# Kernel tuning notes

Hardware: AMD Instinct MI355X
Metric: run time of the kernel (lower is better)

Reference implementation:

```python
import jax, jax.numpy as jnp
import numpy as np

D_MODEL = 512
PROJ = 2 * D_MODEL  # 1024
N_STATES = 32
KSIZE = 4
LN_EPS = 1e-3  # keras LayerNormalization default epsilon


def setup_inputs() -> dict:
    key = jax.random.key(0)
    ks = jax.random.split(key, 16)
    B, L = 2, 2048
    s_in = 1.0 / np.sqrt(D_MODEL)
    s_pr = 1.0 / np.sqrt(PROJ)
    x = jax.random.normal(ks[0], (B, L, D_MODEL), dtype=jnp.float32)
    # LayerNorm params
    ln_gamma = jnp.ones((D_MODEL,), jnp.float32)
    ln_beta = jnp.zeros((D_MODEL,), jnp.float32)
    # dense1 / dense2: d_model -> proj
    W1 = jax.random.normal(ks[1], (D_MODEL, PROJ), jnp.float32) * s_in
    b1 = jnp.zeros((PROJ,), jnp.float32)
    W2 = jax.random.normal(ks[2], (D_MODEL, PROJ), jnp.float32) * s_in
    b2 = jnp.zeros((PROJ,), jnp.float32)
    # depthwise causal conv1d: kernel (K, 1, PROJ) in WIO layout, groups=PROJ
    conv_k = jax.random.normal(ks[3], (KSIZE, 1, PROJ), jnp.float32) * 0.5
    conv_b = jnp.zeros((PROJ,), jnp.float32)
    # SSM params
    A_log = jnp.log(jnp.broadcast_to(jnp.arange(1, N_STATES + 1, dtype=jnp.float32), (PROJ, N_STATES)))
    D_skip = jnp.ones((PROJ,), jnp.float32)
    WB = jax.random.normal(ks[4], (PROJ, N_STATES), jnp.float32) * s_pr
    bB = jnp.zeros((N_STATES,), jnp.float32)
    WC = jax.random.normal(ks[5], (PROJ, N_STATES), jnp.float32) * s_pr
    bC = jnp.zeros((N_STATES,), jnp.float32)
    Wd = jax.random.normal(ks[6], (PROJ, PROJ), jnp.float32) * s_pr
    bd = jnp.zeros((PROJ,), jnp.float32)
    # dense3: proj -> d_model
    W3 = jax.random.normal(ks[7], (PROJ, D_MODEL), jnp.float32) * s_pr
    b3 = jnp.zeros((D_MODEL,), jnp.float32)
    return dict(x=x, ln_gamma=ln_gamma, ln_beta=ln_beta, W1=W1, b1=b1, W2=W2, b2=b2,
                conv_k=conv_k, conv_b=conv_b, A_log=A_log, D_skip=D_skip,
                WB=WB, bB=bB, WC=WC, bC=bC, Wd=Wd, bd=bd, W3=W3, b3=b3)


def _layernorm(x, gamma, beta):
    mu = jnp.mean(x, axis=-1, keepdims=True)
    var = jnp.mean(jnp.square(x - mu), axis=-1, keepdims=True)
    return (x - mu) * jax.lax.rsqrt(var + LN_EPS) * gamma + beta


def _causal_dwconv(x, k, b):
    # x: [B,L,C], k: [K,1,C], depthwise causal conv (left-pad K-1)
    y = jax.lax.conv_general_dilated(
        x, k, window_strides=(1,), padding=[(KSIZE - 1, 0)],
        dimension_numbers=('NWC', 'WIO', 'NWC'), feature_group_count=PROJ)
    return y + b


def _selective_scan(u, delta, A, Bm, Cm, D_skip):
    # u, delta: [B,L,D]; A: [D,N]; Bm, Cm: [B,L,N]; D_skip: [D]
    deltaA = jnp.einsum('bld,dn->bldn', delta, A)                 # [B,L,D,N]
    deltaBu = jnp.einsum('bld,bld,bln->bldn', delta, u, Bm)        # [B,L,D,N]
    # shift deltaA left by one along L, zero at the end (pad trick in source)
    shifted = jnp.concatenate([deltaA[:, 1:], jnp.zeros_like(deltaA[:, :1])], axis=1)
    # reversed cumsum along L, then exp
    e = jnp.exp(jnp.flip(jnp.cumsum(jnp.flip(shifted, axis=1), axis=1), axis=1))
    xs = jnp.cumsum(deltaBu * e, axis=1) / (e + 1e-12)
    y = jnp.einsum('bldn,bln->bld', xs, Cm)
    return y + u * D_skip


def reference(x, ln_gamma, ln_beta, W1, b1, W2, b2, conv_k, conv_b,
              A_log, D_skip, WB, bB, WC, bC, Wd, bd, W3, b3):
    h = _layernorm(x, ln_gamma, ln_beta)
    x1 = h @ W1 + b1                      # [B,L,PROJ]
    x1 = _causal_dwconv(x1, conv_k, conv_b)
    x1 = jax.nn.silu(x1)
    A = -jnp.exp(A_log)                    # [PROJ,N]
    Cm = x1 @ WC + bC                      # [B,L,N]
    Bm = x1 @ WB + bB                      # [B,L,N]
    delta = jax.nn.softplus(x1 @ Wd + bd)  # [B,L,PROJ]
    y = _selective_scan(x1, delta, A, Bm, Cm, D_skip)
    x2 = jax.nn.silu(h @ W2 + b2)
    out = (y * x2) @ W3 + b3 + x           # residual; dropout is identity at inference
    return out
```

## Files before the change

### kernel.cpp

```cpp
#include <hip/hip_runtime.h>
#include <stdint.h>

#define L_SEQ 2048
#define BATCH 2
#define DMODEL 512
#define PROJ 1024
#define NST 32
#define NCATU 1088
#define ROWS (BATCH*L_SEQ)
#define THRESH 50.0f

typedef float f32x4 __attribute__((ext_vector_type(4)));
typedef short short8 __attribute__((ext_vector_type(8)));

__device__ inline float bf2f(unsigned short u){ uint32_t x=((uint32_t)u)<<16; float f; __builtin_memcpy(&f,&x,4); return f; }
__device__ inline unsigned short f2bf(float f){ uint32_t x; __builtin_memcpy(&x,&f,4); uint32_t r=x+0x7FFFu+((x>>16)&1u); return (unsigned short)(r>>16); }
__device__ inline float siluf(float x){ return x/(1.f+__expf(-x)); }
__device__ inline float softplusf(float x){ return x>20.f? x : log1pf(__expf(x)); }

#define AS1(p) ((const __attribute__((address_space(1))) void*)(p))
#define AS3(p) ((__attribute__((address_space(3))) void*)(p))

template<int N> __device__ inline void wait_vmcnt(){
  if constexpr (N==0)      asm volatile("s_waitcnt vmcnt(0)" ::: "memory");
  else if constexpr (N==4) asm volatile("s_waitcnt vmcnt(4)" ::: "memory");
  else if constexpr (N==8) asm volatile("s_waitcnt vmcnt(8)" ::: "memory");
  else                     asm volatile("s_waitcnt vmcnt(12)" ::: "memory");
}

__global__ __launch_bounds__(256)
void prep_ln_kernel(const float* __restrict__ W1, const float* __restrict__ b1,
                    const float* __restrict__ W2, const float* __restrict__ b2,
                    const float* __restrict__ Wd, const float* __restrict__ bd,
                    const float* __restrict__ WB, const float* __restrict__ bB,
                    const float* __restrict__ WC, const float* __restrict__ bC,
                    const float* __restrict__ W3,
                    unsigned short* __restrict__ W12t, unsigned short* __restrict__ Wcatt,
                    unsigned short* __restrict__ W3t, float* __restrict__ bias12,
                    float* __restrict__ biascat,
                    const float* __restrict__ x, const float* __restrict__ ln_g,
                    const float* __restrict__ ln_b, unsigned short* __restrict__ H)
{
  __shared__ float tile[32][33];
  int bid = blockIdx.x;
  int lx = threadIdx.x & 31, ly = threadIdx.x >> 5;
  if (bid < 1024) {
    int kt = bid & 15, nt = bid >> 4;
    int k0 = kt*32, n0 = nt*32;
    const float* S = (n0 < 1024) ? W1 : W2;
    int nc = (n0 < 1024) ? n0 : n0 - 1024;
#pragma unroll
    for (int i=0;i<4;i++)
      tile[ly+i*8][lx] = S[(size_t)(k0+ly+i*8)*1024 + nc + lx];
    __syncthreads();
#pragma unroll
    for (int i=0;i<4;i++)
      W12t[(size_t)(n0+ly+i*8)*512 + k0 + lx] = f2bf(tile[lx][ly+i*8]);
    return;
  }
  if (bid < 2112) {
    int t = bid - 1024;
    int kt = t & 31, nt = t >> 5;
    int k0 = kt*32, n0 = nt*32;
#pragma unroll
    for (int i=0;i<4;i++){
      int k = k0 + ly + i*8;
      float v;
      if (n0 < 1024)       v = Wd[(size_t)k*1024 + n0 + lx];
      else if (n0 == 1024) v = WB[(size_t)k*32 + lx];
      else                 v = WC[(size_t)k*32 + lx];
      tile[ly+i*8][lx] = v;
    }
    __syncthreads();
#pragma unroll
    for (int i=0;i<4;i++)
      Wcatt[(size_t)(n0+ly+i*8)*1024 + k0 + lx] = f2bf(tile[lx][ly+i*8]);
    return;
  }
  if (bid < 2624) {
    int t = bid - 2112;
    int kt = t & 31, nt = t >> 5;
    int k0 = kt*32, n0 = nt*32;
#pragma unroll
    for (int i=0;i<4;i++)
      tile[ly+i*8][lx] = W3[(size_t)(k0+ly+i*8)*512 + n0 + lx];
    __syncthreads();
#pragma unroll
    for (int i=0;i<4;i++)
      W3t[(size_t)(n0+ly+i*8)*1024 + k0 + lx] = f2bf(tile[lx][ly+i*8]);
    return;
  }
  if (bid < 2637) {
    int j = (bid - 2624)*256 + threadIdx.x;
    if (j < 2048) { bias12[j] = (j < 1024) ? b1[j] : b2[j-1024]; return; }
    j -= 2048;
    if (j < NCATU) biascat[j] = (j < 1024) ? bd[j] : (j < 1056) ? bB[j-1024] : bC[j-1056];
    return;
  }
  int row = (bid - 2637)*4 + (threadIdx.x >> 6);
  int lane = threadIdx.x & 63;
  const float4* xr = (const float4*)(x + (size_t)row*DMODEL);
  float4 v0 = xr[lane];
  float4 v1 = xr[lane+64];
  float s = v0.x+v0.y+v0.z+v0.w + v1.x+v1.y+v1.z+v1.w;
  float q = v0.x*v0.x+v0.y*v0.y+v0.z*v0.z+v0.w*v0.w
          + v1.x*v1.x+v1.y*v1.y+v1.z*v1.z+v1.w*v1.w;
#pragma unroll
  for (int m=32;m>0;m>>=1){ s += __shfl_xor(s,m); q += __shfl_xor(q,m); }
  float mu = s*(1.f/DMODEL);
  float var = q*(1.f/DMODEL) - mu*mu;
  float rs = rsqrtf(var + 1e-3f);
  int c0 = lane*4, c1 = 256 + lane*4;
  float4 g0 = *(const float4*)&ln_g[c0]; float4 g1 = *(const float4*)&ln_g[c1];
  float4 t0 = *(const float4*)&ln_b[c0]; float4 t1 = *(const float4*)&ln_b[c1];
  ushort4 o0, o1;
  o0.x = f2bf((v0.x-mu)*rs*g0.x + t0.x);
  o0.y = f2bf((v0.y-mu)*rs*g0.y + t0.y);
  o0.z = f2bf((v0.z-mu)*rs*g0.z + t0.z);
  o0.w = f2bf((v0.w-mu)*rs*g0.w + t0.w);
  o1.x = f2bf((v1.x-mu)*rs*g1.x + t1.x);
  o1.y = f2bf((v1.y-mu)*rs*g1.y + t1.y);
  o1.z = f2bf((v1.z-mu)*rs*g1.z + t1.z);
  o1.w = f2bf((v1.w-mu)*rs*g1.w + t1.w);
  *(ushort4*)&H[(size_t)row*DMODEL + c0] = o0;
  *(ushort4*)&H[(size_t)row*DMODEL + c1] = o1;
}

__global__ __launch_bounds__(256)
void gemm128_g1(const unsigned short* __restrict__ A, const unsigned short* __restrict__ Bt,
                unsigned short* __restrict__ P12n, unsigned short* __restrict__ x2bf,
                const float* __restrict__ bias, int M, int N, int K)
{
  constexpr int BK = 64;
  constexpr int LPT = 8;
  __shared__ unsigned short As[2][128*BK];
  __shared__ unsigned short Bs[2][128*BK];
  int tid = threadIdx.x;
  int lane = tid & 63, wid = tid >> 6;
  int wm = wid >> 1, wn = wid & 1;
  int gx = gridDim.x;
  int nwg = gx * gridDim.y;
  int L = blockIdx.y*gx + blockIdx.x;
  int W = (L & 7)*(nwg >> 3) + (L >> 3);
  int bx = W % gx, by = W / gx;
  int m0 = bx*128, n0 = by*128;

  f32x4 acc[4][4];
#pragma unroll
  for (int i=0;i<4;i++)
#pragma unroll
    for (int j=0;j<4;j++)
#pragma unroll
      for (int e=0;e<4;e++) acc[i][j][e] = 0.f;

  const unsigned short* ap[4];
  const unsigned short* bp[4];
#pragma unroll
  for (int j=0;j<4;j++){
    int s = tid + j*256;
    int row = s >> 3, kc = ((s & 7) ^ (row & 7)) * 8;
    ap[j] = A + (size_t)(m0+row)*K + kc;
    bp[j] = Bt + (size_t)(n0+row)*K + kc;
  }
  auto stage = [&](int buf){
#pragma unroll
    for (int j=0;j<4;j++){
      __builtin_amdgcn_global_load_lds(AS1(ap[j]), AS3(&As[buf][(size_t)(j*256 + wid*64)*8]), 16, 0, 0);
      ap[j] += BK;
    }
#pragma unroll
    for (int j=0;j<4;j++){
      __builtin_amdgcn_global_load_lds(AS1(bp[j]), AS3(&Bs[buf][(size_t)(j*256 + wid*64)*8]), 16, 0, 0);
      bp[j] += BK;
    }
  };
  stage(0);
  stage(1);
  int T = K/BK;
  int r = lane & 15, kb = lane >> 4;
  for (int t = 0; t < T; ++t) {
    int rb = t & 1;
    if (t+1 < T) wait_vmcnt<LPT>();
    else         wait_vmcnt<0>();
    __builtin_amdgcn_s_barrier();
    short8 af[2][4], bfr[2][4];
#pragma unroll
    for (int ks=0; ks<2; ++ks) {
      int cx = (ks*4 + kb) ^ (r & 7);
#pragma unroll
      for (int i=0;i<4;i++) af[ks][i]  = *(const short8*)&As[rb][((wm*64 + i*16 + r)*8 + cx)*8];
#pragma unroll
      for (int j=0;j<4;j++) bfr[ks][j] = *(const short8*)&Bs[rb][((wn*64 + j*16 + r)*8 + cx)*8];
    }
    asm volatile("s_waitcnt lgkmcnt(0)" ::: "memory");
    __builtin_amdgcn_sched_barrier(0);
    __builtin_amdgcn_s_barrier();
    if (t+2 < T) stage(rb);
    __builtin_amdgcn_s_setprio(1);
#pragma unroll
    for (int ks=0; ks<2; ++ks)
#pragma unroll
      for (int i=0;i<4;i++)
#pragma unroll
        for (int j=0;j<4;j++)
          acc[i][j] = __builtin_amdgcn_mfma_f32_16x16x32_bf16(af[ks][i], bfr[ks][j], acc[i][j], 0,0,0);
    __builtin_amdgcn_s_setprio(0);
  }

  int rr = (lane >> 4)*4, cc = lane & 15;
#pragma unroll
  for (int i=0;i<4;i++)
#pragma unroll
    for (int j=0;j<4;j++) {
      int col = n0 + wn*64 + j*16 + cc;
      float bcol = bias[col];
#pragma unroll
      for (int e=0;e<4;e++) {
        int row = m0 + wm*64 + i*16 + rr + e;
        float v = acc[i][j][e] + bcol;
        if (col < 1024) P12n[(size_t)row*1024 + col] = f2bf(v);
        else            x2bf[(size_t)row*1024 + col - 1024] = f2bf(siluf(v));
      }
    }
}

template<int MODE>
__global__ __launch_bounds__(256)
void gemm64(const unsigned short* __restrict__ A, const unsigned short* __restrict__ Bt,
            void* __restrict__ Cv, const float* __restrict__ bias,
            int M, int N, int K, int Kfull)
{
  constexpr int BK = 64;
  constexpr int LPT = 4;
  __shared__ unsigned short As[3][64*BK];
  __shared__ unsigned short Bs[3][64*BK];
  int tid = threadIdx.x;
  int lane = tid & 63, wid = tid >> 6;
  int wm = wid >> 1, wn = wid & 1;
  int gx = gridDim.x;
  int nwg = gx * gridDim.y;
  int L = blockIdx.y*gx + blockIdx.x;
  int W = (L & 7)*(nwg >> 3) + (L >> 3);
  int bx = W % gx, by = W / gx;
  int m0 = bx*64, n0 = by*64;
  int kofs = blockIdx.z*K;

  f32x4 acc[2][2];
#pragma unroll
  for (int i=0;i<2;i++)
#pragma unroll
    for (int j=0;j<2;j++)
#pragma unroll
      for (int e=0;e<4;e++) acc[i][j][e] = 0.f;

  const unsigned short* ap[2];
  const unsigned short* bp[2];
#pragma unroll
  for (int j=0;j<2;j++){
    int s = tid + j*256;
    int row = s >> 3, kc = ((s & 7) ^ (row & 7)) * 8;
    ap[j] = A + (size_t)(m0+row)*Kfull + kofs + kc;
    bp[j] = Bt + (size_t)(n0+row)*Kfull + kofs + kc;
  }
  auto stage = [&](int buf){
#pragma unroll
    for (int j=0;j<2;j++){
      __builtin_amdgcn_global_load_lds(AS1(ap[j]), AS3(&As[buf][(size_t)(j*256 + wid*64)*8]), 16, 0, 0);
      ap[j] += BK;
    }
#pragma unroll
    for (int j=0;j<2;j++){
      __builtin_amdgcn_global_load_lds(AS1(bp[j]), AS3(&Bs[buf][(size_t)(j*256 + wid*64)*8]), 16, 0, 0);
      bp[j] += BK;
    }
  };
  stage(0); stage(1);
  int T = K/BK;
  int rb = 0, wb = 2;
  int r = lane & 15, kb = lane >> 4;
  for (int t = 0; t < T; ++t) {
    if (t+1 < T) wait_vmcnt<LPT>();
    else         wait_vmcnt<0>();
    __builtin_amdgcn_s_barrier();
    if (t+2 < T) { stage(wb); wb = (wb==2)?0:wb+1; }
#pragma unroll
    for (int ks=0; ks<2; ++ks) {
      int cx = (ks*4 + kb) ^ (r & 7);
      short8 af[2], bfr[2];
#pragma unroll
      for (int i=0;i<2;i++) af[i]  = *(const short8*)&As[rb][((wm*32 + i*16 + r)*8 + cx)*8];
#pragma unroll
      for (int j=0;j<2;j++) bfr[j] = *(const short8*)&Bs[rb][((wn*32 + j*16 + r)*8 + cx)*8];
      __builtin_amdgcn_s_setprio(1);
#pragma unroll
      for (int i=0;i<2;i++)
#pragma unroll
        for (int j=0;j<2;j++)
          acc[i][j] = __builtin_amdgcn_mfma_f32_16x16x32_bf16(af[i], bfr[j], acc[i][j], 0,0,0);
      __builtin_amdgcn_s_setprio(0);
    }
    rb = (rb==2)?0:rb+1;
  }
  int rr = (lane >> 4)*4, cc = lane & 15;
#pragma unroll
  for (int i=0;i<2;i++)
#pragma unroll
    for (int j=0;j<2;j++) {
      int col = n0 + wn*32 + j*16 + cc;
#pragma unroll
      for (int e=0;e<4;e++) {
        int row = m0 + wm*32 + i*16 + rr + e;
        float v = acc[i][j][e];
        if constexpr (MODE == 2) {
          v += bias[row];
          if (row < 1024) v = softplusf(v);
          ((float*)Cv)[(size_t)row*N + col] = v;
        } else {
          ((float*)Cv)[(size_t)blockIdx.z*M*N + (size_t)row*N + col] = v;
        }
      }
    }
}

__global__ __launch_bounds__(256)
void reduce_kernel(const float* __restrict__ P, const float* __restrict__ x,
                   const float* __restrict__ b3, float* __restrict__ out)
{
  size_t i = ((size_t)blockIdx.x*256 + threadIdx.x)*4;
  int col = (int)(i & 511);
  float4 a = *(const float4*)&P[i];
  float4 b = *(const float4*)&P[(size_t)ROWS*512 + i];
  float4 xv = *(const float4*)&x[i];
  float4 bv = *(const float4*)&b3[col];
  float4 o;
  o.x = a.x + b.x + xv.x + bv.x;
  o.y = a.y + b.y + xv.y + bv.y;
  o.z = a.z + b.z + xv.z + bv.z;
  o.w = a.w + b.w + xv.w + bv.w;
  *(float4*)&out[i] = o;
}

__global__ __launch_bounds__(256)
void conv_silu_kernel(const unsigned short* __restrict__ P12n, const float* __restrict__ ck,
                      const float* __restrict__ cb, unsigned short* __restrict__ ubf)
{
  int gid = blockIdx.x*256 + threadIdx.x;
  int c = (gid & 255)*4;
  int row = gid >> 8;
  int l = row & (L_SEQ-1);
  float4 bv = *(const float4*)&cb[c];
  float r0=bv.x, r1=bv.y, r2=bv.z, r3=bv.w;
#pragma unroll
  for (int t=0;t<4;t++){
    int lsrc = l - 3 + t;
    if (lsrc >= 0) {
      ushort4 xv = *(const ushort4*)&P12n[(size_t)(row-3+t)*1024 + c];
      float4 kv = *(const float4*)&ck[t*PROJ + c];
      r0 = fmaf(bf2f(xv.x),kv.x,r0);
      r1 = fmaf(bf2f(xv.y),kv.y,r1);
      r2 = fmaf(bf2f(xv.z),kv.z,r2);
      r3 = fmaf(bf2f(xv.w),kv.w,r3);
    }
  }
  ushort4 o;
  o.x=f2bf(siluf(r0)); o.y=f2bf(siluf(r1)); o.z=f2bf(siluf(r2)); o.w=f2bf(siluf(r3));
  *(ushort4*)&ubf[(size_t)row*PROJ + c] = o;
}

__global__ __launch_bounds__(256)
void zmul_pre_kernel(const unsigned short* __restrict__ ubf, const unsigned short* __restrict__ x2bf,
                     const float* __restrict__ Dskip, unsigned short* __restrict__ zbf)
{
  size_t i = ((size_t)blockIdx.x*256 + threadIdx.x)*4;
  int d = (int)(i & (PROJ-1));
  ushort4 uu = *(const ushort4*)&ubf[i];
  ushort4 xx = *(const ushort4*)&x2bf[i];
  float4 Dv = *(const float4*)&Dskip[d];
  ushort4 o;
  o.x = f2bf(bf2f(uu.x)*Dv.x*bf2f(xx.x));
  o.y = f2bf(bf2f(uu.y)*Dv.y*bf2f(xx.y));
  o.z = f2bf(bf2f(uu.z)*Dv.z*bf2f(xx.z));
  o.w = f2bf(bf2f(uu.w)*Dv.w*bf2f(xx.w));
  *(ushort4*)&zbf[i] = o;
}

__global__ __launch_bounds__(256)
void sscan_kernel(const float* __restrict__ CT, const unsigned short* __restrict__ ubf,
                  const unsigned short* __restrict__ x2bf, const float* __restrict__ Dskip,
                  const float* __restrict__ A_log, unsigned short* __restrict__ zbf)
{
  __shared__ float suf8sh[8][256];
  int tid = threadIdx.x;
  int n = tid & 31, gsub = tid >> 5;
  int G = blockIdx.x*8 + gsub;
  int b = G >> 10, d = G & 1023;
  const float* dT = CT + (size_t)d*ROWS + b*L_SEQ;

  float mysum = 0.f;
  {
    const float4* c4 = (const float4*)(dT + n*64);
    for (int it=0; it<16; ++it){ float4 v = c4[it]; mysum += v.x+v.y+v.z+v.w; }
  }
  float incl = mysum;
#pragma unroll
  for (int dlt=1; dlt<32; dlt<<=1){ float t = __shfl_up(incl, dlt, 32); if (n >= dlt) incl += t; }
  float Tot = __shfl(incl, 31, 32);
  float excl = incl - mysum;
  int cnt = 0;
  {
    const float4* c4 = (const float4*)(dT + n*64);
    float run = excl;
    for (int it=0; it<16; ++it){
      float4 v = c4[it];
      if ((it & 1) == 0) suf8sh[gsub][n*8 + (it>>1)] = Tot - run;
      cnt += (Tot - run >= THRESH); run += v.x;
      cnt += (Tot - run >= THRESH); run += v.y;
      cnt += (Tot - run >= THRESH); run += v.z;
      cnt += (Tot - run >= THRESH); run += v.w;
    }
  }
#pragma unroll
  for (int m=16;m>0;m>>=1) cnt += __shfl_xor(cnt, m, 32);
  int myl0 = cnt > 0 ? cnt-1 : 0;
  __syncthreads();

  int base = min(myl0, __shfl_xor(myl0, 32)) & ~7;
  float np1 = __expf(A_log[d*NST + n]);
  float Ds = Dskip[d];
  const float* Br = CT + (size_t)(1024+n)*ROWS + b*L_SEQ;
  const float* Cr = CT + (size_t)(1056+n)*ROWS + b*L_SEQ;
  const unsigned short* ub = ubf + (size_t)b*L_SEQ*PROJ + d;
  const unsigned short* xb = x2bf + (size_t)b*L_SEQ*PROJ + d;
  unsigned short* zb = zbf + (size_t)b*L_SEQ*PROJ + d;
  float s = 0.f;
  for (int l = base; l < L_SEQ; l += 8) {
    float4 d0 = *(const float4*)&dT[l];
    float4 d1 = *(const float4*)&dT[l+4];
    float4 B0 = *(const float4*)&Br[l];
    float4 B1 = *(const float4*)&Br[l+4];
    float4 C0 = *(const float4*)&Cr[l];
    float4 C1 = *(const float4*)&Cr[l+4];
    float sufv = suf8sh[gsub][l >> 3];
    float dl[8] = {d0.x,d0.y,d0.z,d0.w,d1.x,d1.y,d1.z,d1.w};
    float Bv[8] = {B0.x,B0.y,B0.z,B0.w,B1.x,B1.y,B1.z,B1.w};
    float Cv[8] = {C0.x,C0.y,C0.z,C0.w,C1.x,C1.y,C1.z,C1.w};
    float uu[8];
#pragma unroll
    for (int t=0;t<8;t++) uu[t] = bf2f(ub[(size_t)(l+t)*PROJ]);
    float cum = 0.f;
#pragma unroll
    for (int t=0;t<8;t++){
      cum += dl[t];
      float decay = __expf(-dl[t]*np1);
      s = fmaf(decay, s, dl[t]*uu[t]*Bv[t]);
      float gte = 1.f/(1.f + 1e-12f*__expf(np1*(sufv - cum)));
      float contrib = s*gte*Cv[t];
#pragma unroll
      for (int m=16;m>0;m>>=1) contrib += __shfl_xor(contrib, m);
      if (n == 0) {
        float x2v = bf2f(xb[(size_t)(l+t)*PROJ]);
        zb[(size_t)(l+t)*PROJ] = f2bf((contrib + uu[t]*Ds)*x2v);
      }
    }
  }
}

extern "C" void kernel_launch(void* const* d_in, const int* in_sizes, int n_in,
                              void* d_out, int out_size, void* d_ws, size_t ws_size,
                              hipStream_t stream)
{
  const float* x     = (const float*)d_in[0];
  const float* ln_g  = (const float*)d_in[1];
  const float* ln_b  = (const float*)d_in[2];
  const float* W1    = (const float*)d_in[3];
  const float* b1    = (const float*)d_in[4];
  const float* W2    = (const float*)d_in[5];
  const float* b2    = (const float*)d_in[6];
  const float* convk = (const float*)d_in[7];
  const float* convb = (const float*)d_in[8];
  const float* A_log = (const float*)d_in[9];
  const float* Dskip = (const float*)d_in[10];
  const float* WB    = (const float*)d_in[11];
  const float* bB    = (const float*)d_in[12];
  const float* WC    = (const float*)d_in[13];
  const float* bC    = (const float*)d_in[14];
  const float* Wd    = (const float*)d_in[15];
  const float* bd    = (const float*)d_in[16];
  const float* W3    = (const float*)d_in[17];
  const float* b3    = (const float*)d_in[18];

  char* w = (char*)d_ws;
  auto alloc = [&](size_t bytes){ char* p = w; w += (bytes + 255) & ~(size_t)255; return p; };
  unsigned short* Hbf    = (unsigned short*)alloc((size_t)ROWS*DMODEL*2);
  unsigned short* W12t   = (unsigned short*)alloc((size_t)2048*512*2);
  unsigned short* Wcatt  = (unsigned short*)alloc((size_t)NCATU*1024*2);
  unsigned short* W3t    = (unsigned short*)alloc((size_t)512*1024*2);
  float*          bias12 = (float*)alloc(2048*4);
  float*          biascat= (float*)alloc(NCATU*4);
  unsigned short* P12n   = (unsigned short*)alloc((size_t)ROWS*1024*2);
  unsigned short* ubf    = (unsigned short*)alloc((size_t)ROWS*PROJ*2);
  unsigned short* x2bf   = (unsigned short*)alloc((size_t)ROWS*PROJ*2);
  float*          CT     = (float*)alloc((size_t)NCATU*ROWS*4);
  unsigned short* zbf    = (unsigned short*)alloc((size_t)ROWS*PROJ*2);
  float*          Pp     = (float*)alloc((size_t)2*ROWS*512*4);

  prep_ln_kernel<<<3661, 256, 0, stream>>>(W1,b1,W2,b2,Wd,bd,WB,bB,WC,bC,W3,
                                           W12t,Wcatt,W3t,bias12,biascat,
                                           x, ln_g, ln_b, Hbf);

  dim3 g1(ROWS/128, 2048/128);
  gemm128_g1<<<g1, 256, 0, stream>>>(Hbf, W12t, P12n, x2bf, bias12, ROWS, 2048, DMODEL);

  conv_silu_kernel<<<ROWS*256/256, 256, 0, stream>>>(P12n, convk, convb, ubf);

  zmul_pre_kernel<<<(ROWS*PROJ/4)/256, 256, 0, stream>>>(ubf, x2bf, Dskip, zbf);

  dim3 g2(NCATU/64, ROWS/64);
  gemm64<2><<<g2, 256, 0, stream>>>(Wcatt, ubf, CT, biascat, NCATU, ROWS, PROJ, PROJ);

  sscan_kernel<<<2048/8, 256, 0, stream>>>(CT, ubf, x2bf, Dskip, A_log, zbf);

  dim3 g3(ROWS/64, 512/64, 2);
  gemm64<5><<<g3, 256, 0, stream>>>(zbf, W3t, Pp, b3, ROWS, 512, 512, PROJ);
  reduce_kernel<<<(ROWS*512/4)/256, 256, 0, stream>>>(Pp, x, b3, (float*)d_out);
}
```

Before: 162.9 us.

## Run first projection GEMM with 64x64 tiles and hoist x2 loads in scan

Removes the dedicated 128x128-tile GEMM for the LN-to-W1/W2 projection and reuses the 64x64-tile gemm64 template with a new MODE 1 epilogue, which applies the bias, writes the conv input and silu(x2) in bf16, and launches four times as many workgroups. Separately, the selective-scan kernel now loads the eight x2 values per step up front alongside u instead of inside the n==0 branch of the inner loop. The smaller tile raises occupancy and CU coverage for a K=512 GEMM but lowers data reuse per tile. The hoisted loads are now issued by all lanes rather than only n==0 lanes, trading extra loads for less latency on the serial path.

```diff
diff --git a/kernel.cpp b/kernel.cpp
--- a/kernel.cpp
+++ b/kernel.cpp
@@ -126,108 +126,10 @@
   *(ushort4*)&H[(size_t)row*DMODEL + c1] = o1;
 }
 
-__global__ __launch_bounds__(256)
-void gemm128_g1(const unsigned short* __restrict__ A, const unsigned short* __restrict__ Bt,
-                unsigned short* __restrict__ P12n, unsigned short* __restrict__ x2bf,
-                const float* __restrict__ bias, int M, int N, int K)
-{
-  constexpr int BK = 64;
-  constexpr int LPT = 8;
-  __shared__ unsigned short As[2][128*BK];
-  __shared__ unsigned short Bs[2][128*BK];
-  int tid = threadIdx.x;
-  int lane = tid & 63, wid = tid >> 6;
-  int wm = wid >> 1, wn = wid & 1;
-  int gx = gridDim.x;
-  int nwg = gx * gridDim.y;
-  int L = blockIdx.y*gx + blockIdx.x;
-  int W = (L & 7)*(nwg >> 3) + (L >> 3);
-  int bx = W % gx, by = W / gx;
-  int m0 = bx*128, n0 = by*128;
-
-  f32x4 acc[4][4];
-#pragma unroll
-  for (int i=0;i<4;i++)
-#pragma unroll
-    for (int j=0;j<4;j++)
-#pragma unroll
-      for (int e=0;e<4;e++) acc[i][j][e] = 0.f;
-
-  const unsigned short* ap[4];
-  const unsigned short* bp[4];
-#pragma unroll
-  for (int j=0;j<4;j++){
-    int s = tid + j*256;
-    int row = s >> 3, kc = ((s & 7) ^ (row & 7)) * 8;
-    ap[j] = A + (size_t)(m0+row)*K + kc;
-    bp[j] = Bt + (size_t)(n0+row)*K + kc;
-  }
-  auto stage = [&](int buf){
-#pragma unroll
-    for (int j=0;j<4;j++){
-      __builtin_amdgcn_global_load_lds(AS1(ap[j]), AS3(&As[buf][(size_t)(j*256 + wid*64)*8]), 16, 0, 0);
-      ap[j] += BK;
-    }
-#pragma unroll
-    for (int j=0;j<4;j++){
-      __builtin_amdgcn_global_load_lds(AS1(bp[j]), AS3(&Bs[buf][(size_t)(j*256 + wid*64)*8]), 16, 0, 0);
-      bp[j] += BK;
-    }
-  };
-  stage(0);
-  stage(1);
-  int T = K/BK;
-  int r = lane & 15, kb = lane >> 4;
-  for (int t = 0; t < T; ++t) {
-    int rb = t & 1;
-    if (t+1 < T) wait_vmcnt<LPT>();
-    else         wait_vmcnt<0>();
-    __builtin_amdgcn_s_barrier();
-    short8 af[2][4], bfr[2][4];
-#pragma unroll
-    for (int ks=0; ks<2; ++ks) {
-      int cx = (ks*4 + kb) ^ (r & 7);
-#pragma unroll
-      for (int i=0;i<4;i++) af[ks][i]  = *(const short8*)&As[rb][((wm*64 + i*16 + r)*8 + cx)*8];
-#pragma unroll
-      for (int j=0;j<4;j++) bfr[ks][j] = *(const short8*)&Bs[rb][((wn*64 + j*16 + r)*8 + cx)*8];
-    }
-    asm volatile("s_waitcnt lgkmcnt(0)" ::: "memory");
-    __builtin_amdgcn_sched_barrier(0);
-    __builtin_amdgcn_s_barrier();
-    if (t+2 < T) stage(rb);
-    __builtin_amdgcn_s_setprio(1);
-#pragma unroll
-    for (int ks=0; ks<2; ++ks)
-#pragma unroll
-      for (int i=0;i<4;i++)
-#pragma unroll
-        for (int j=0;j<4;j++)
-          acc[i][j] = __builtin_amdgcn_mfma_f32_16x16x32_bf16(af[ks][i], bfr[ks][j], acc[i][j], 0,0,0);
-    __builtin_amdgcn_s_setprio(0);
-  }
-
-  int rr = (lane >> 4)*4, cc = lane & 15;
-#pragma unroll
-  for (int i=0;i<4;i++)
-#pragma unroll
-    for (int j=0;j<4;j++) {
-      int col = n0 + wn*64 + j*16 + cc;
-      float bcol = bias[col];
-#pragma unroll
-      for (int e=0;e<4;e++) {
-        int row = m0 + wm*64 + i*16 + rr + e;
-        float v = acc[i][j][e] + bcol;
-        if (col < 1024) P12n[(size_t)row*1024 + col] = f2bf(v);
-        else            x2bf[(size_t)row*1024 + col - 1024] = f2bf(siluf(v));
-      }
-    }
-}
-
 template<int MODE>
 __global__ __launch_bounds__(256)
 void gemm64(const unsigned short* __restrict__ A, const unsigned short* __restrict__ Bt,
-            void* __restrict__ Cv, const float* __restrict__ bias,
+            void* __restrict__ Cv, void* __restrict__ Cv2, const float* __restrict__ bias,
             int M, int N, int K, int Kfull)
 {
   constexpr int BK = 64;
@@ -311,7 +213,11 @@
       for (int e=0;e<4;e++) {
         int row = m0 + wm*32 + i*16 + rr + e;
         float v = acc[i][j][e];
-        if constexpr (MODE == 2) {
+        if constexpr (MODE == 1) {
+          v += bias[col];
+          if (col < 1024) ((unsigned short*)Cv)[(size_t)row*1024 + col] = f2bf(v);
+          else            ((unsigned short*)Cv2)[(size_t)row*1024 + col - 1024] = f2bf(siluf(v));
+        } else if constexpr (MODE == 2) {
           v += bias[row];
           if (row < 1024) v = softplusf(v);
           ((float*)Cv)[(size_t)row*N + col] = v;
@@ -440,13 +346,15 @@
     float4 B1 = *(const float4*)&Br[l+4];
     float4 C0 = *(const float4*)&Cr[l];
     float4 C1 = *(const float4*)&Cr[l+4];
+    float uu[8], xx[8];
+#pragma unroll
+    for (int t=0;t<8;t++) uu[t] = bf2f(ub[(size_t)(l+t)*PROJ]);
+#pragma unroll
+    for (int t=0;t<8;t++) xx[t] = bf2f(xb[(size_t)(l+t)*PROJ]);
     float sufv = suf8sh[gsub][l >> 3];
     float dl[8] = {d0.x,d0.y,d0.z,d0.w,d1.x,d1.y,d1.z,d1.w};
     float Bv[8] = {B0.x,B0.y,B0.z,B0.w,B1.x,B1.y,B1.z,B1.w};
     float Cv[8] = {C0.x,C0.y,C0.z,C0.w,C1.x,C1.y,C1.z,C1.w};
-    float uu[8];
-#pragma unroll
-    for (int t=0;t<8;t++) uu[t] = bf2f(ub[(size_t)(l+t)*PROJ]);
     float cum = 0.f;
 #pragma unroll
     for (int t=0;t<8;t++){
@@ -457,10 +365,8 @@
       float contrib = s*gte*Cv[t];
 #pragma unroll
       for (int m=16;m>0;m>>=1) contrib += __shfl_xor(contrib, m);
-      if (n == 0) {
-        float x2v = bf2f(xb[(size_t)(l+t)*PROJ]);
-        zb[(size_t)(l+t)*PROJ] = f2bf((contrib + uu[t]*Ds)*x2v);
-      }
+      if (n == 0)
+        zb[(size_t)(l+t)*PROJ] = f2bf((contrib + uu[t]*Ds)*xx[t]);
     }
   }
 }
@@ -508,19 +414,19 @@
                                            W12t,Wcatt,W3t,bias12,biascat,
                                            x, ln_g, ln_b, Hbf);
 
-  dim3 g1(ROWS/128, 2048/128);
-  gemm128_g1<<<g1, 256, 0, stream>>>(Hbf, W12t, P12n, x2bf, bias12, ROWS, 2048, DMODEL);
+  dim3 g1(ROWS/64, 2048/64);
+  gemm64<1><<<g1, 256, 0, stream>>>(Hbf, W12t, P12n, x2bf, bias12, ROWS, 2048, DMODEL, DMODEL);
 
   conv_silu_kernel<<<ROWS*256/256, 256, 0, stream>>>(P12n, convk, convb, ubf);
 
   zmul_pre_kernel<<<(ROWS*PROJ/4)/256, 256, 0, stream>>>(ubf, x2bf, Dskip, zbf);
 
   dim3 g2(NCATU/64, ROWS/64);
-  gemm64<2><<<g2, 256, 0, stream>>>(Wcatt, ubf, CT, biascat, NCATU, ROWS, PROJ, PROJ);
+  gemm64<2><<<g2, 256, 0, stream>>>(Wcatt, ubf, CT, nullptr, biascat, NCATU, ROWS, PROJ, PROJ);
 
   sscan_kernel<<<2048/8, 256, 0, stream>>>(CT, ubf, x2bf, Dskip, A_log, zbf);
 
   dim3 g3(ROWS/64, 512/64, 2);
-  gemm64<5><<<g3, 256, 0, stream>>>(zbf, W3t, Pp, b3, ROWS, 512, 512, PROJ);
+  gemm64<5><<<g3, 256, 0, stream>>>(zbf, W3t, Pp, nullptr, b3, ROWS, 512, 512, PROJ);
   reduce_kernel<<<(ROWS*512/4)/256, 256, 0, stream>>>(Pp, x, b3, (float*)d_out);
 }
```

After: 154.9 us. 1.05x faster.
